# Kernel tuning notes

Measured on AMD Instinct MI355X. Metric: run time of the kernel, lower is better.

## Reference

```python
import jax, jax.numpy as jnp
import numpy as np

B, T, F = 256, 192, 8
CARD0, CARD1 = 1000, 100
E0, E1 = 32, 16
H = 512
D_IN = F + E0 + E1  # 56


def _glorot(key, shape):
    fan_in, fan_out = shape[0], shape[-1]
    lim = jnp.sqrt(6.0 / (fan_in + fan_out))
    return jax.random.uniform(key, shape, jnp.float32, -lim, lim)


def setup_inputs() -> dict:
    key = jax.random.key(0)
    ks = jax.random.split(key, 16)
    return {
        "x_cont": jax.random.normal(ks[0], (B, T, F), jnp.float32),
        "cat0": jax.random.randint(ks[1], (B, T), 0, CARD0),
        "cat1": jax.random.randint(ks[2], (B, T), 0, CARD1),
        "emb0": _glorot(ks[3], (CARD0, E0)),
        "emb1": _glorot(ks[4], (CARD1, E1)),
        "Wk1": _glorot(ks[5], (D_IN, 4 * H)),
        "Wr1": _glorot(ks[6], (H, 4 * H)),
        "b1": jnp.zeros((4 * H,), jnp.float32).at[H:2 * H].set(1.0),  # unit_forget_bias
        "Wk2": _glorot(ks[7], (H, 4 * H)),
        "Wr2": _glorot(ks[8], (H, 4 * H)),
        "b2": jnp.zeros((4 * H,), jnp.float32).at[H:2 * H].set(1.0),
        "Wmu": _glorot(ks[9], (H, 1)),
        "bmu": _glorot(ks[10], (1, 1))[0],
        "Wsig": _glorot(ks[11], (H, 1)),
        "bsig": _glorot(ks[12], (1, 1))[0],
    }


def _lstm(x, Wk, Wr, b):
    # x: [B, T, D]; Keras gate order i, f, g(c), o; zero initial states (inference mode,
    # dropout/recurrent_dropout inactive when training=False).
    xz = jnp.einsum('btd,dk->btk', x, Wk) + b  # precompute input projection for all steps
    h0 = jnp.zeros((x.shape[0], H), x.dtype)

    def step(carry, z_t):
        h, c = carry
        z = z_t + h @ Wr  # [B, 4H]
        i, f, g, o = jnp.split(z, 4, axis=-1)
        i = jax.nn.sigmoid(i)
        f = jax.nn.sigmoid(f)
        g = jnp.tanh(g)
        o = jax.nn.sigmoid(o)
        c = f * c + i * g
        h = o * jnp.tanh(c)
        return (h, c), h

    _, hs = jax.lax.scan(step, (h0, h0), jnp.swapaxes(xz, 0, 1))  # [T, B, H]
    return jnp.swapaxes(hs, 0, 1)


def reference(x_cont, cat0, cat1, emb0, emb1, Wk1, Wr1, b1, Wk2, Wr2, b2, Wmu, bmu, Wsig, bsig):
    x = jnp.concatenate([x_cont, emb0[cat0], emb1[cat1]], axis=-1)  # [B, T, 56]
    x = _lstm(x, Wk1, Wr1, b1)
    x = _lstm(x, Wk2, Wr2, b2)
    mu = x @ Wmu + bmu                      # count_data=False -> raw mu
    sigma = jax.nn.softplus(x @ Wsig + bsig)
    return (mu, sigma)
```

## Files before the change

kernel.cpp:

```cpp
#include <hip/hip_runtime.h>
#include <math.h>

#define Bsz 256
#define Tsz 192
#define Fc 8
#define E0c 32
#define E1c 16
#define Hc 512
#define G4 2048
#define DINP 64
#define K1t 576
#define K2t 1024
#define NBLK 256
#define LBLK 32
#define KPAD1 584
#define KPAD2 1032
#define LDSB_BYTES (64 * KPAD2 * 2)
#define SLOT_STRIDE 16
#define DEP_OFF (32 * SLOT_STRIDE)
#define PF_BLOCK (64 * SLOT_STRIDE)
#define WD_WAIT (1 << 17)

typedef __attribute__((ext_vector_type(8))) short short8;
typedef __attribute__((ext_vector_type(4))) float f32x4;

template<int N> struct IC { static constexpr int v = N; };
template<int C, int CMAX, typename F>
__device__ __forceinline__ void static_for(F&& f) {
    if constexpr (C < CMAX) {
        f(IC<C>{});
        static_for<C + 1, CMAX>(f);
    }
}

static __device__ __forceinline__ float bf2f(ushort u) {
    return __uint_as_float(((uint)u) << 16);
}
static __device__ __forceinline__ ushort f2bf(float f) {
    uint u = __float_as_uint(f);
    u = (u + 0x7fffu + ((u >> 16) & 1u)) >> 16;
    return (ushort)u;
}

static __device__ __forceinline__ uint poll_sc1(const uint* p) {
    uint v;
    asm volatile("global_load_dword %0, %1, off sc1\n\t"
                 "s_waitcnt vmcnt(0)"
                 : "=v"(v) : "v"((unsigned long long)p) : "memory");
    return v;
}
static __device__ __forceinline__ void store_slot_sc1(uint* p, uint v) {
    asm volatile("global_store_dword %0, %1, off sc1"
                 :: "v"((unsigned long long)p), "v"(v) : "memory");
}

__global__ __launch_bounds__(256) void build_x_kernel(
    const float* __restrict__ x_cont, const int* __restrict__ cat0,
    const int* __restrict__ cat1, const float* __restrict__ emb0,
    const float* __restrict__ emb1, ushort* __restrict__ x_bf)
{
    int idx = blockIdx.x * 256 + threadIdx.x;
    if (idx >= Tsz * Bsz * DINP) return;
    int d = idx & 63;
    int row = idx >> 6;
    int t = row >> 8;
    int b = row & 255;
    float v = 0.f;
    if (d < Fc)                  v = x_cont[(b * Tsz + t) * Fc + d];
    else if (d < Fc + E0c)       v = emb0[cat0[b * Tsz + t] * E0c + (d - Fc)];
    else if (d < Fc + E0c + E1c) v = emb1[cat1[b * Tsz + t] * E1c + (d - Fc - E0c)];
    x_bf[idx] = f2bf(v);
}

__global__ __launch_bounds__(256) void transpose_w_kernel(
    const float* __restrict__ in, ushort* __restrict__ out, int K, int ldout, int coff)
{
    __shared__ float tile[32][33];
    int k0 = blockIdx.x * 32;
    int n0 = blockIdx.y * 32;
    int tx = threadIdx.x & 31, ty = threadIdx.x >> 5;
    #pragma unroll
    for (int p = 0; p < 4; ++p) {
        int k = k0 + ty + p * 8;
        tile[ty + p * 8][tx] = (k < K) ? in[k * G4 + n0 + tx] : 0.f;
    }
    __syncthreads();
    #pragma unroll
    for (int p = 0; p < 4; ++p) {
        int nl = ty + p * 8;
        out[(size_t)(n0 + nl) * ldout + coff + k0 + tx] = f2bf(tile[tx][nl]);
    }
}

static __device__ __forceinline__ void wait_slots(const uint* arr, uint tg) {
    const uint* p = arr + (threadIdx.x & 31) * SLOT_STRIDE;
    int it = 0;
    while (true) {
        uint v = poll_sc1(p);
        if (__all((int)(v >= tg))) break;
        if (++it >= WD_WAIT) break;
        __builtin_amdgcn_s_sleep(1);
    }
}

template<int KS_IN, int KS_TOT, int LDA_IN, int KPADv, bool HAS_DEP, int FANOUT>
static __device__ __forceinline__ void run_layer(
    const ushort* __restrict__ Ain,
    ushort* __restrict__ hbuf,
    const ushort* __restrict__ hz,
    const ushort* __restrict__ Wt,
    const float* __restrict__ bias,
    ushort* B_lds,
    uint* pflags,
    int g, int jb, int m0, int j0)
{
    constexpr int KS_R = KS_TOT - KS_IN;
    constexpr int KL = KS_TOT * 32;
    constexpr int SEGS = KL / 8;
    int tid = threadIdx.x;
    int lane = tid & 63, wv = tid >> 6;
    int lane15 = lane & 15, quad = lane >> 4;
    int bid = jb * 8 + g * 2 + (HAS_DEP ? 1 : 0);

    const uint* own_arr = pflags + bid * PF_BLOCK;
    const uint* dep_arr = own_arr + DEP_OFF;

    uint* pub_dst = nullptr;
    if (tid < FANOUT) {
        int j = tid & 31;
        int cons_role = (HAS_DEP ? 1 : (tid >> 5));
        int cons_bid = j * 8 + g * 2 + cons_role;
        pub_dst = pflags + cons_bid * PF_BLOCK + ((tid >> 5) ? DEP_OFF : 0)
                + jb * SLOT_STRIDE;
    }

    for (int i = tid; i < 64 * SEGS; i += 256) {
        int row = i / SEGS, seg = i - row * SEGS;
        int gz = (row >> 4) * Hc + j0 + (row & 15);
        *(uint4*)&B_lds[row * KPADv + seg * 8] =
            *(const uint4*)(Wt + (size_t)gz * KL + seg * 8);
    }
    __syncthreads();

    float bgate[4];
    #pragma unroll
    for (int gt = 0; gt < 4; ++gt) bgate[gt] = bias[gt * Hc + j0 + lane15];
    float cst[4] = {0.f, 0.f, 0.f, 0.f};

    int arow = m0 + wv * 16 + lane15;
    int crow0 = m0 + wv * 16 + quad * 4;

    for (int t = 0; t < Tsz; ++t) {
        f32x4 acc[4];
        #pragma unroll
        for (int gt = 0; gt < 4; ++gt) acc[gt] = (f32x4){0.f, 0.f, 0.f, 0.f};

        if constexpr (HAS_DEP) {
            if (tid < 64) wait_slots(dep_arr, (uint)(t + 1));
            __syncthreads();
        }
        {
            const ushort* p0 = Ain + ((size_t)t * Bsz + arow) * LDA_IN + quad * 8;
            uint4 bufA[KS_IN];
            static_for<0, KS_IN>([&](auto Kc) {
                constexpr int ks = decltype(Kc)::v;
                bufA[ks] = *(const uint4*)(p0 + ks * 32);
            });
            asm volatile("" ::: "memory");
            static_for<0, KS_IN>([&](auto Kc) {
                constexpr int ks = decltype(Kc)::v;
                short8 av = __builtin_bit_cast(short8, bufA[ks]);
                #pragma unroll
                for (int gt = 0; gt < 4; ++gt) {
                    short8 bfr = *(const short8*)&B_lds[(gt * 16 + lane15) * KPADv + ks * 32 + quad * 8];
                    acc[gt] = __builtin_amdgcn_mfma_f32_16x16x32_bf16(av, bfr, acc[gt], 0, 0, 0);
                }
            });
        }

        if (t) {
            if (tid < 64) wait_slots(own_arr, (uint)t);
            __syncthreads();
        }
        {
            const ushort* p1base = (t > 0) ? (hbuf + (size_t)(t - 1) * Bsz * Hc) : hz;
            const ushort* p1 = p1base + (size_t)arow * Hc + quad * 8;
            uint4 bufB[KS_R];
            static_for<0, KS_R>([&](auto Kc) {
                constexpr int ks = decltype(Kc)::v;
                bufB[ks] = *(const uint4*)(p1 + ks * 32);
            });
            asm volatile("" ::: "memory");
            static_for<0, KS_R>([&](auto Kc) {
                constexpr int ks = decltype(Kc)::v;
                short8 av = __builtin_bit_cast(short8, bufB[ks]);
                #pragma unroll
                for (int gt = 0; gt < 4; ++gt) {
                    short8 bfr = *(const short8*)&B_lds[(gt * 16 + lane15) * KPADv + (KS_IN + ks) * 32 + quad * 8];
                    acc[gt] = __builtin_amdgcn_mfma_f32_16x16x32_bf16(av, bfr, acc[gt], 0, 0, 0);
                }
            });
        }

        uint hv[4];
        #pragma unroll
        for (int r = 0; r < 4; ++r) {
            float zi = acc[0][r] + bgate[0];
            float zf = acc[1][r] + bgate[1];
            float zg = acc[2][r] + bgate[2];
            float zo = acc[3][r] + bgate[3];
            float ig = 1.f / (1.f + __expf(-zi));
            float fg = 1.f / (1.f + __expf(-zf));
            float gg = tanhf(zg);
            float og = 1.f / (1.f + __expf(-zo));
            float cn = fg * cst[r] + ig * gg;
            cst[r] = cn;
            float hn = og * tanhf(cn);
            hv[r] = (uint)f2bf(hn);
        }
        {
            unsigned long long hb = (unsigned long long)
                &hbuf[((size_t)t * Bsz + crow0) * Hc + j0 + lane15];
            asm volatile(
                "global_store_short %0, %1, off sc1\n\t"
                "global_store_short %0, %2, off offset:1024 sc1\n\t"
                "global_store_short %0, %3, off offset:2048 sc1\n\t"
                "global_store_short %0, %4, off offset:3072 sc1\n\t"
                "s_waitcnt vmcnt(0)"
                :: "v"(hb), "v"(hv[0]), "v"(hv[1]), "v"(hv[2]), "v"(hv[3])
                : "memory");
        }

        __syncthreads();
        if (tid < FANOUT)
            store_slot_sc1(pub_dst, (uint)(t + 1));
    }
}

__global__ __launch_bounds__(256, 1) void deepar_persistent(
    const ushort* __restrict__ x_bf,
    const ushort* __restrict__ Wt1, const ushort* __restrict__ Wt2,
    const float* __restrict__ b1, const float* __restrict__ b2,
    ushort* __restrict__ h1, ushort* __restrict__ h2,
    const ushort* __restrict__ hz,
    const float* __restrict__ Wmu, const float* __restrict__ bmu,
    const float* __restrict__ Wsig, const float* __restrict__ bsig,
    float* __restrict__ out, uint* __restrict__ pflags)
{
    extern __shared__ ushort B_lds[];

    int bid = blockIdx.x;
    int xcd = bid & 7;
    int g = xcd >> 1;
    int role = xcd & 1;
    int jb = bid >> 3;
    int m0 = g * 64;
    int j0 = jb * 16;

    if (role == 0) {
        run_layer<2, 18, DINP, KPAD1, false, 64>(x_bf, h1, hz, Wt1, b1, B_lds,
                                                 pflags, g, jb, m0, j0);
        return;
    }
    run_layer<16, 32, Hc, KPAD2, true, 32>(h1, h2, hz, Wt2, b2, B_lds,
                                           pflags, g, jb, m0, j0);

    const uint* own_arr = pflags + bid * PF_BLOCK;
    if (threadIdx.x < 64) wait_slots(own_arr, (uint)Tsz);
    __syncthreads();

    int lane = threadIdx.x & 63, wv = threadIdx.x >> 6;
    float wm[8], wsg[8];
    #pragma unroll
    for (int i = 0; i < 8; ++i) {
        wm[i] = Wmu[lane * 8 + i];
        wsg[i] = Wsig[lane * 8 + i];
    }
    float bmu0 = bmu[0], bsg0 = bsig[0];
    for (int i = jb * 4 + wv; i < 64 * Tsz; i += 128) {
        int b = m0 + (i & 63);
        int t = i >> 6;
        const ushort* hp = h2 + ((size_t)t * Bsz + b) * Hc + lane * 8;
        short8 hvv = *(const short8*)hp;
        float smu = 0.f, ssg = 0.f;
        #pragma unroll
        for (int e = 0; e < 8; ++e) {
            float f = bf2f((ushort)hvv[e]);
            smu += f * wm[e];
            ssg += f * wsg[e];
        }
        #pragma unroll
        for (int off = 32; off > 0; off >>= 1) {
            smu += __shfl_down(smu, off, 64);
            ssg += __shfl_down(ssg, off, 64);
        }
        if (lane == 0) {
            int oi = b * Tsz + t;
            float sg = ssg + bsg0;
            float sp = sg > 0.f ? sg + log1pf(__expf(-sg)) : log1pf(__expf(sg));
            out[oi] = smu + bmu0;
            out[Bsz * Tsz + oi] = sp;
        }
    }
}

extern "C" void kernel_launch(void* const* d_in, const int* in_sizes, int n_in,
                              void* d_out, int out_size, void* d_ws, size_t ws_size,
                              hipStream_t stream) {
    const float* x_cont = (const float*)d_in[0];
    const int*   cat0   = (const int*)d_in[1];
    const int*   cat1   = (const int*)d_in[2];
    const float* emb0   = (const float*)d_in[3];
    const float* emb1   = (const float*)d_in[4];
    const float* Wk1    = (const float*)d_in[5];
    const float* Wr1    = (const float*)d_in[6];
    const float* b1     = (const float*)d_in[7];
    const float* Wk2    = (const float*)d_in[8];
    const float* Wr2    = (const float*)d_in[9];
    const float* b2     = (const float*)d_in[10];
    const float* Wmu    = (const float*)d_in[11];
    const float* bmu    = (const float*)d_in[12];
    const float* Wsig   = (const float*)d_in[13];
    const float* bsig   = (const float*)d_in[14];
    float* out = (float*)d_out;

    const size_t pflags_bytes = (size_t)NBLK * PF_BLOCK * 4;

    char* ws = (char*)d_ws;
    uint*   pflags = (uint*)ws;                                ws += pflags_bytes;
    ushort* x_bf  = (ushort*)ws;                               ws += (size_t)Tsz * Bsz * DINP * 2;
    ushort* Wt1   = (ushort*)ws;                               ws += (size_t)G4 * K1t * 2;
    ushort* Wt2   = (ushort*)ws;                               ws += (size_t)G4 * K2t * 2;
    ushort* h1    = (ushort*)ws;                               ws += (size_t)Tsz * Bsz * Hc * 2;
    ushort* h2    = (ushort*)ws;                               ws += (size_t)Tsz * Bsz * Hc * 2;
    ushort* hz    = (ushort*)ws;                               ws += (size_t)Bsz * Hc * 2;

    hipMemsetAsync(pflags, 0, pflags_bytes, stream);
    hipMemsetAsync(hz, 0, (size_t)Bsz * Hc * 2, stream);

    build_x_kernel<<<(Tsz * Bsz * DINP + 255) / 256, 256, 0, stream>>>(
        x_cont, cat0, cat1, emb0, emb1, x_bf);
    transpose_w_kernel<<<dim3(2, 64), 256, 0, stream>>>(Wk1, Wt1, 56, K1t, 0);
    transpose_w_kernel<<<dim3(16, 64), 256, 0, stream>>>(Wr1, Wt1, Hc, K1t, DINP);
    transpose_w_kernel<<<dim3(16, 64), 256, 0, stream>>>(Wk2, Wt2, Hc, K2t, 0);
    transpose_w_kernel<<<dim3(16, 64), 256, 0, stream>>>(Wr2, Wt2, Hc, K2t, Hc);

    hipFuncSetAttribute((const void*)deepar_persistent,
                        hipFuncAttributeMaxDynamicSharedMemorySize, LDSB_BYTES);
    deepar_persistent<<<dim3(NBLK), dim3(256), LDSB_BYTES, stream>>>(
        x_bf, Wt1, Wt2, b1, b2, h1, h2, hz, Wmu, bmu, Wsig, bsig, out, pflags);
}
```

Before: 1.360 ms.

## Replace block-level flag sync with per-wavefront flag rings

```diff
diff --git a/kernel.cpp b/kernel.cpp
--- a/kernel.cpp
+++ b/kernel.cpp
@@ -12,13 +12,11 @@
 #define K1t 576
 #define K2t 1024
 #define NBLK 256
-#define LBLK 32
 #define KPAD1 584
 #define KPAD2 1032
 #define LDSB_BYTES (64 * KPAD2 * 2)
 #define SLOT_STRIDE 16
-#define DEP_OFF (32 * SLOT_STRIDE)
-#define PF_BLOCK (64 * SLOT_STRIDE)
+#define RING_U (64 * SLOT_STRIDE)
 #define WD_WAIT (1 << 17)
 
 typedef __attribute__((ext_vector_type(8))) short short8;
@@ -122,16 +120,17 @@
     int lane15 = lane & 15, quad = lane >> 4;
     int bid = jb * 8 + g * 2 + (HAS_DEP ? 1 : 0);
 
-    const uint* own_arr = pflags + bid * PF_BLOCK;
-    const uint* dep_arr = own_arr + DEP_OFF;
-
-    uint* pub_dst = nullptr;
-    if (tid < FANOUT) {
-        int j = tid & 31;
-        int cons_role = (HAS_DEP ? 1 : (tid >> 5));
+    uint* ring = pflags + (size_t)(bid * 4 + wv) * RING_U;
+    const uint* own_arr = ring;
+    const uint* dep_arr = ring + 32 * SLOT_STRIDE;
+
+    uint* pub_dst;
+    {
+        int j = lane & 31;
+        int cons_role = HAS_DEP ? 1 : (lane >> 5);
         int cons_bid = j * 8 + g * 2 + cons_role;
-        pub_dst = pflags + cons_bid * PF_BLOCK + ((tid >> 5) ? DEP_OFF : 0)
-                + jb * SLOT_STRIDE;
+        pub_dst = pflags + (size_t)(cons_bid * 4 + wv) * RING_U
+                + ((lane >= 32) ? 32 * SLOT_STRIDE : 0) + jb * SLOT_STRIDE;
     }
 
     for (int i = tid; i < 64 * SEGS; i += 256) {
@@ -156,8 +155,7 @@
         for (int gt = 0; gt < 4; ++gt) acc[gt] = (f32x4){0.f, 0.f, 0.f, 0.f};
 
         if constexpr (HAS_DEP) {
-            if (tid < 64) wait_slots(dep_arr, (uint)(t + 1));
-            __syncthreads();
+            wait_slots(dep_arr, (uint)(t + 1));
         }
         {
             const ushort* p0 = Ain + ((size_t)t * Bsz + arow) * LDA_IN + quad * 8;
@@ -178,10 +176,7 @@
             });
         }
 
-        if (t) {
-            if (tid < 64) wait_slots(own_arr, (uint)t);
-            __syncthreads();
-        }
+        if (t) wait_slots(own_arr, (uint)t);
         {
             const ushort* p1base = (t > 0) ? (hbuf + (size_t)(t - 1) * Bsz * Hc) : hz;
             const ushort* p1 = p1base + (size_t)arow * Hc + quad * 8;
@@ -230,9 +225,7 @@
                 :: "v"(hb), "v"(hv[0]), "v"(hv[1]), "v"(hv[2]), "v"(hv[3])
                 : "memory");
         }
-
-        __syncthreads();
-        if (tid < FANOUT)
+        if (lane < FANOUT)
             store_slot_sc1(pub_dst, (uint)(t + 1));
     }
 }
@@ -265,8 +258,11 @@
     run_layer<16, 32, Hc, KPAD2, true, 32>(h1, h2, hz, Wt2, b2, B_lds,
                                            pflags, g, jb, m0, j0);
 
-    const uint* own_arr = pflags + bid * PF_BLOCK;
-    if (threadIdx.x < 64) wait_slots(own_arr, (uint)Tsz);
+    {
+        int wv = threadIdx.x >> 6;
+        const uint* ring = pflags + (size_t)(bid * 4 + wv) * RING_U;
+        wait_slots(ring, (uint)Tsz);
+    }
     __syncthreads();
 
     int lane = threadIdx.x & 63, wv = threadIdx.x >> 6;
@@ -324,7 +320,7 @@
     const float* bsig   = (const float*)d_in[14];
     float* out = (float*)d_out;
 
-    const size_t pflags_bytes = (size_t)NBLK * PF_BLOCK * 4;
+    const size_t pflags_bytes = (size_t)NBLK * 4 * RING_U * 4;
 
     char* ws = (char*)d_ws;
     uint*   pflags = (uint*)ws;                                ws += pflags_bytes;
```

New measurement: 1.195 ms. 12.2% less time.
